# Kernel tuning notes

Measured on AMD Instinct MI355X. Metric: run time of the kernel, lower is better.

The kernel has to match this reference:

```python
import jax, jax.numpy as jnp
import numpy as np

NUM_CLASSES = 19  # configer.get('data','num_classes')


def _batch_label_vector(targets, num_classes, grid_size):
    # targets: [B, H, W] int labels in [0, num_classes)
    b, h, w = targets.shape
    pad_h = (-h) % grid_size
    pad_w = (-w) % grid_size
    # pad with value == num_classes, which torch.histc(min=0, max=num_classes-1)
    # ignores; we route it to an extra dustbin column and drop it.
    t = jnp.pad(targets, ((0, 0), (0, pad_h), (0, pad_w)),
                constant_values=num_classes)
    hh, ww = h + pad_h, w + pad_w
    # tile into (grid_size x grid_size) blocks -> [n_blocks, g*g]
    t = t.reshape(b, hh // grid_size, grid_size, ww // grid_size, grid_size)
    t = t.transpose(0, 1, 3, 2, 4).reshape(-1, grid_size * grid_size)
    n_blocks = t.shape[0]
    rows = jnp.arange(n_blocks)[:, None]  # [n_blocks, 1]
    # presence vector: hist > 0 <=> scatter-set ones at (block, label)
    tvect = jnp.zeros((n_blocks, num_classes + 1), jnp.float32)
    tvect = tvect.at[rows, t].set(1.0)
    return tvect[:, :num_classes]  # drop dustbin (pad value) column


def setup_inputs() -> dict:
    key = jax.random.key(0)
    k1, k2 = jax.random.split(key)
    B, H, W, G = 16, 1024, 2048, 8
    n_blocks = B * (H // G) * (W // G)  # 524288
    preds = jax.random.normal(k1, (n_blocks, NUM_CLASSES), jnp.float32)
    targets = jax.random.randint(k2, (B, H, W), 0, NUM_CLASSES, jnp.int32)
    return {"preds": preds, "targets": targets, "grid_size": G}


def reference(preds, targets, grid_size):
    se_target = _batch_label_vector(targets, NUM_CLASSES, grid_size)
    # BCELoss(sigmoid(preds), se_target), mean reduction.
    # Numerically stable: -log(sigmoid(x)) = softplus(-x),
    #                     -log(1-sigmoid(x)) = softplus(x)
    loss = se_target * jax.nn.softplus(-preds) + (1.0 - se_target) * jax.nn.softplus(preds)
    return jnp.mean(loss)
```

## Files before the change

### kernel.cpp

```cpp
#include <hip/hip_runtime.h>
#include <cmath>


typedef float uf4 __attribute__((vector_size(16), aligned(4)));

__global__ __launch_bounds__(256) void fsenc_loss_kernel(
    const float* __restrict__ preds,
    const int*   __restrict__ targets,
    float*       __restrict__ out,
    int B, int H, int W, float inv_count)
{
    const int t  = threadIdx.x;
    const int wg = blockIdx.x;

    const int strips_per_row = W / 1024;
    const int rows_per_img   = H / 8;
    const int block_row = wg / strips_per_row;
    const int strip     = wg % strips_per_row;
    const int b_img = block_row / rows_per_img;
    const int bh    = block_row % rows_per_img;
    const int col0  = strip * 1024;

    const int4* tgt4 = (const int4*)targets;
    const long row_stride4 = (long)W / 4;
    const long tbase = ((long)(b_img * H + bh * 8) * W + col0) / 4 + t;

    int4 tv[8];
    #pragma unroll
    for (int r = 0; r < 8; ++r)
        tv[r] = tgt4[tbase + (long)r * row_stride4];

    const long row = (long)wg * 2432 + (long)(t >> 1) * 19;
    const float* p = preds + row;
    uf4 q0 = {0.f, 0.f, 0.f, 0.f}, q1 = q0, q2 = q0;
    if ((t & 1) == 0) {
        q0 = *(const uf4*)(p + 0);
        q1 = *(const uf4*)(p + 4);
    } else {
        q0 = *(const uf4*)(p + 8);
        q1 = *(const uf4*)(p + 12);
        q2 = *(const uf4*)(p + 15);
    }

    unsigned mask = 0u;
    #pragma unroll
    for (int r = 0; r < 8; ++r)
        mask |= (1u << tv[r].x) | (1u << tv[r].y) | (1u << tv[r].z) | (1u << tv[r].w);
    mask |= __shfl_xor(mask, 1);

    float acc = 0.f;
    #define SP_TERM(xval, cls)                                                 \
        {                                                                      \
            float x_ = (xval);                                                 \
            float sp_ = fmaxf(x_, 0.f) + __logf(1.f + __expf(-fabsf(x_)));     \
            acc += sp_ - (float)((mask >> (cls)) & 1u) * x_;                   \
        }
    if ((t & 1) == 0) {
        SP_TERM(q0[0], 0)  SP_TERM(q0[1], 1)  SP_TERM(q0[2], 2)  SP_TERM(q0[3], 3)
        SP_TERM(q1[0], 4)  SP_TERM(q1[1], 5)  SP_TERM(q1[2], 6)  SP_TERM(q1[3], 7)
    } else {
        SP_TERM(q0[0], 8)  SP_TERM(q0[1], 9)  SP_TERM(q0[2], 10) SP_TERM(q0[3], 11)
        SP_TERM(q1[0], 12) SP_TERM(q1[1], 13) SP_TERM(q1[2], 14) SP_TERM(q1[3], 15)
        SP_TERM(q2[1], 16) SP_TERM(q2[2], 17) SP_TERM(q2[3], 18)
    }
    #undef SP_TERM

    #pragma unroll
    for (int off = 32; off; off >>= 1)
        acc += __shfl_down(acc, off);

    __shared__ float s_part[4];
    if ((t & 63) == 0) s_part[t >> 6] = acc;
    __syncthreads();
    if (t == 0) {
        float tot = s_part[0] + s_part[1] + s_part[2] + s_part[3];
        atomicAdd(out, tot * inv_count);
    }
}

extern "C" void kernel_launch(void* const* d_in, const int* in_sizes, int n_in,
                              void* d_out, int out_size, void* d_ws, size_t ws_size,
                              hipStream_t stream) {
    const float* preds   = (const float*)d_in[0];
    const int*   targets = (const int*)d_in[1];
    float*       out     = (float*)d_out;

    const int B = 16, H = 1024, W = 2048;
    const float inv_count = 1.0f / (float)in_sizes[0];

    (void)hipMemsetAsync(out, 0, sizeof(float), stream);

    const int grid = B * (H / 8) * (W / 1024);
    fsenc_loss_kernel<<<grid, 256, 0, stream>>>(preds, targets, out,
                                                B, H, W, inv_count);
}
```

Measured before the change: 223.3 us.

## Process full 8-row bands per workgroup with two blocks per thread pair and nontemporal loads

Each workgroup now covers a whole 8-row band of 2048 columns (256 grid blocks) instead of a 1024-column strip, halving the grid and giving every thread pair two 8x8 blocks. Targets and preds are read with nontemporal loads because they are streamed once. The extra in-flight loads per thread are meant to raise memory-level parallelism and cut per-workgroup overhead and atomics, at the cost of more registers and fewer workgroups to spread across CUs.

```diff
diff --git a/kernel.cpp b/kernel.cpp
--- a/kernel.cpp
+++ b/kernel.cpp
@@ -2,66 +2,73 @@
 #include <cmath>
 
 
-typedef float uf4 __attribute__((vector_size(16), aligned(4)));
+typedef int   i4v __attribute__((ext_vector_type(4), aligned(16)));
+typedef float f4u __attribute__((ext_vector_type(4), aligned(4)));
 
 __global__ __launch_bounds__(256) void fsenc_loss_kernel(
     const float* __restrict__ preds,
     const int*   __restrict__ targets,
     float*       __restrict__ out,
-    int B, int H, int W, float inv_count)
+    float inv_count)
 {
-    const int t  = threadIdx.x;
-    const int wg = blockIdx.x;
+    const int t    = threadIdx.x;
+    const int band = blockIdx.x;
 
-    const int strips_per_row = W / 1024;
-    const int rows_per_img   = H / 8;
-    const int block_row = wg / strips_per_row;
-    const int strip     = wg % strips_per_row;
-    const int b_img = block_row / rows_per_img;
-    const int bh    = block_row % rows_per_img;
-    const int col0  = strip * 1024;
-
-    const int4* tgt4 = (const int4*)targets;
-    const long row_stride4 = (long)W / 4;
-    const long tbase = ((long)(b_img * H + bh * 8) * W + col0) / 4 + t;
-
-    int4 tv[8];
+    const i4v* tb = (const i4v*)targets + (long)band * 4096;
+    i4v tv[16];
     #pragma unroll
-    for (int r = 0; r < 8; ++r)
-        tv[r] = tgt4[tbase + (long)r * row_stride4];
-
-    const long row = (long)wg * 2432 + (long)(t >> 1) * 19;
-    const float* p = preds + row;
-    uf4 q0 = {0.f, 0.f, 0.f, 0.f}, q1 = q0, q2 = q0;
-    if ((t & 1) == 0) {
-        q0 = *(const uf4*)(p + 0);
-        q1 = *(const uf4*)(p + 4);
-    } else {
-        q0 = *(const uf4*)(p + 8);
-        q1 = *(const uf4*)(p + 12);
-        q2 = *(const uf4*)(p + 15);
+    for (int r = 0; r < 8; ++r) {
+        tv[2*r]   = __builtin_nontemporal_load(tb + r * 512 + t);
+        tv[2*r+1] = __builtin_nontemporal_load(tb + r * 512 + t + 256);
     }
 
-    unsigned mask = 0u;
+    const long blockA = (long)band * 256 + (t >> 1);
+    const float* pA = preds + blockA * 19;
+    const float* pB = pA + 128 * 19;
+    f4u a0 = {0.f,0.f,0.f,0.f}, a1 = a0, a2 = a0, b0 = a0, b1 = a0, b2 = a0;
+    if ((t & 1) == 0) {
+        a0 = __builtin_nontemporal_load((const f4u*)(pA + 0));
+        a1 = __builtin_nontemporal_load((const f4u*)(pA + 4));
+        b0 = __builtin_nontemporal_load((const f4u*)(pB + 0));
+        b1 = __builtin_nontemporal_load((const f4u*)(pB + 4));
+    } else {
+        a0 = __builtin_nontemporal_load((const f4u*)(pA + 8));
+        a1 = __builtin_nontemporal_load((const f4u*)(pA + 12));
+        a2 = __builtin_nontemporal_load((const f4u*)(pA + 15));
+        b0 = __builtin_nontemporal_load((const f4u*)(pB + 8));
+        b1 = __builtin_nontemporal_load((const f4u*)(pB + 12));
+        b2 = __builtin_nontemporal_load((const f4u*)(pB + 15));
+    }
+
+    unsigned m0 = 0u, m1 = 0u;
     #pragma unroll
-    for (int r = 0; r < 8; ++r)
-        mask |= (1u << tv[r].x) | (1u << tv[r].y) | (1u << tv[r].z) | (1u << tv[r].w);
-    mask |= __shfl_xor(mask, 1);
+    for (int r = 0; r < 8; ++r) {
+        i4v u = tv[2*r], w = tv[2*r+1];
+        m0 |= (1u << u[0]) | (1u << u[1]) | (1u << u[2]) | (1u << u[3]);
+        m1 |= (1u << w[0]) | (1u << w[1]) | (1u << w[2]) | (1u << w[3]);
+    }
+    m0 |= __shfl_xor(m0, 1);
+    m1 |= __shfl_xor(m1, 1);
 
     float acc = 0.f;
-    #define SP_TERM(xval, cls)                                                 \
+    #define SP_TERM(xval, msk, cls)                                            \
         {                                                                      \
             float x_ = (xval);                                                 \
             float sp_ = fmaxf(x_, 0.f) + __logf(1.f + __expf(-fabsf(x_)));     \
-            acc += sp_ - (float)((mask >> (cls)) & 1u) * x_;                   \
+            acc += sp_ - (float)(((msk) >> (cls)) & 1u) * x_;                  \
         }
     if ((t & 1) == 0) {
-        SP_TERM(q0[0], 0)  SP_TERM(q0[1], 1)  SP_TERM(q0[2], 2)  SP_TERM(q0[3], 3)
-        SP_TERM(q1[0], 4)  SP_TERM(q1[1], 5)  SP_TERM(q1[2], 6)  SP_TERM(q1[3], 7)
+        SP_TERM(a0[0], m0, 0)  SP_TERM(a0[1], m0, 1)  SP_TERM(a0[2], m0, 2)  SP_TERM(a0[3], m0, 3)
+        SP_TERM(a1[0], m0, 4)  SP_TERM(a1[1], m0, 5)  SP_TERM(a1[2], m0, 6)  SP_TERM(a1[3], m0, 7)
+        SP_TERM(b0[0], m1, 0)  SP_TERM(b0[1], m1, 1)  SP_TERM(b0[2], m1, 2)  SP_TERM(b0[3], m1, 3)
+        SP_TERM(b1[0], m1, 4)  SP_TERM(b1[1], m1, 5)  SP_TERM(b1[2], m1, 6)  SP_TERM(b1[3], m1, 7)
     } else {
-        SP_TERM(q0[0], 8)  SP_TERM(q0[1], 9)  SP_TERM(q0[2], 10) SP_TERM(q0[3], 11)
-        SP_TERM(q1[0], 12) SP_TERM(q1[1], 13) SP_TERM(q1[2], 14) SP_TERM(q1[3], 15)
-        SP_TERM(q2[1], 16) SP_TERM(q2[2], 17) SP_TERM(q2[3], 18)
+        SP_TERM(a0[0], m0, 8)  SP_TERM(a0[1], m0, 9)  SP_TERM(a0[2], m0, 10) SP_TERM(a0[3], m0, 11)
+        SP_TERM(a1[0], m0, 12) SP_TERM(a1[1], m0, 13) SP_TERM(a1[2], m0, 14) SP_TERM(a1[3], m0, 15)
+        SP_TERM(a2[1], m0, 16) SP_TERM(a2[2], m0, 17) SP_TERM(a2[3], m0, 18)
+        SP_TERM(b0[0], m1, 8)  SP_TERM(b0[1], m1, 9)  SP_TERM(b0[2], m1, 10) SP_TERM(b0[3], m1, 11)
+        SP_TERM(b1[0], m1, 12) SP_TERM(b1[1], m1, 13) SP_TERM(b1[2], m1, 14) SP_TERM(b1[3], m1, 15)
+        SP_TERM(b2[1], m1, 16) SP_TERM(b2[2], m1, 17) SP_TERM(b2[3], m1, 18)
     }
     #undef SP_TERM
 
@@ -85,12 +92,11 @@
     const int*   targets = (const int*)d_in[1];
     float*       out     = (float*)d_out;
 
-    const int B = 16, H = 1024, W = 2048;
+    const int B = 16, H = 1024;
     const float inv_count = 1.0f / (float)in_sizes[0];
 
     (void)hipMemsetAsync(out, 0, sizeof(float), stream);
 
-    const int grid = B * (H / 8) * (W / 1024);
-    fsenc_loss_kernel<<<grid, 256, 0, stream>>>(preds, targets, out,
-                                                B, H, W, inv_count);
+    const int grid = B * (H / 8);
+    fsenc_loss_kernel<<<grid, 256, 0, stream>>>(preds, targets, out, inv_count);
 }
```

Result: faster. 216.7 us (-3.0%).
